# Optimization experiments

Measured on AMD Instinct MI355X. Metric: run time of the kernel, lower is better.

Reference implementation:

```python
import jax, jax.numpy as jnp
import numpy as np

NUM_HEADS = 16
EMBED_DIM = 1024
HEAD_DIM = EMBED_DIM // NUM_HEADS
DILATION = 4


def setup_inputs() -> dict:
    key = jax.random.key(0)
    ks = jax.random.split(key, 9)
    B, S, E = 2, 4096, EMBED_DIM
    scale = 1.0 / np.sqrt(E)
    inp = {
        "x": jax.random.normal(ks[0], (B, S, E), dtype=jnp.float32),
        "Wq": jax.random.normal(ks[1], (E, E), dtype=jnp.float32) * scale,
        "bq": jnp.zeros((E,), dtype=jnp.float32),
        "Wk": jax.random.normal(ks[2], (E, E), dtype=jnp.float32) * scale,
        "bk": jnp.zeros((E,), dtype=jnp.float32),
        "Wv": jax.random.normal(ks[3], (E, E), dtype=jnp.float32) * scale,
        "bv": jnp.zeros((E,), dtype=jnp.float32),
        "Wo": jax.random.normal(ks[4], (E, E), dtype=jnp.float32) * scale,
        "bo": jnp.zeros((E,), dtype=jnp.float32),
    }
    return inp


def reference(x, Wq, bq, Wk, bk, Wv, bv, Wo, bo):
    B, S, E = x.shape
    H, D = NUM_HEADS, HEAD_DIM

    def split_heads(t):  # [B,S,E] -> [B,H,S,D]
        return t.reshape(B, S, H, D).transpose(0, 2, 1, 3)

    q = split_heads(x @ Wq + bq)
    k = split_heads(x @ Wk + bk)[:, :, ::DILATION, :]   # dilated keys
    v = split_heads(x @ Wv + bv)[:, :, ::DILATION, :]   # dilated values

    scores = jnp.einsum('bhqd,bhkd->bhqk', q, k) / np.sqrt(D).astype(x.dtype)
    attn = jax.nn.softmax(scores, axis=-1)
    ctx = jnp.einsum('bhqk,bhkd->bhqd', attn, v)
    ctx = ctx.transpose(0, 2, 1, 3).reshape(B, S, E)
    return ctx @ Wo + bo
```

## Files before the change

kernel.cpp:

```cpp
#include <hip/hip_runtime.h>
#include <cstdint>
#include <cstddef>

typedef unsigned short u16;
typedef __attribute__((ext_vector_type(4))) float f32x4;
typedef __attribute__((ext_vector_type(8))) short short8;
typedef __attribute__((ext_vector_type(4))) unsigned short u16x4;

#define NH 16
#define ED 1024
#define HD 64
#define SEQ 4096
#define SKV 1024

__device__ __forceinline__ u16 f2bf(float f) {
  unsigned u = __builtin_bit_cast(unsigned, f);
  u += 0x7fffu + ((u >> 16) & 1u);
  return (u16)(u >> 16);
}

__device__ __forceinline__ void gload16(const void* g, void* l) {
  __builtin_amdgcn_global_load_lds((const __attribute__((address_space(1))) void*)g,
                                   (__attribute__((address_space(3))) void*)l, 16, 0, 0);
}

__device__ __forceinline__ f32x4 mfma16(short8 a, short8 b, f32x4 c) {
  return __builtin_amdgcn_mfma_f32_16x16x32_bf16(a, b, c, 0, 0, 0);
}

__global__ __launch_bounds__(256) void prep_kernel(
    const float* __restrict__ x, u16* __restrict__ x16,
    const float* __restrict__ Wq, const float* __restrict__ Wk,
    const float* __restrict__ Wv, const float* __restrict__ Wo,
    u16* __restrict__ Wqt, u16* __restrict__ Wkt,
    u16* __restrict__ Wvt, u16* __restrict__ Wot) {
  __shared__ float t[64][65];
  int bx = blockIdx.x;
  if (bx < 8192) {
    int i = bx * 256 + threadIdx.x;
    f32x4 v = ((const f32x4*)x)[i];
    u16x4 o;
#pragma unroll
    for (int j = 0; j < 4; ++j) o[j] = f2bf(v[j]);
    ((u16x4*)x16)[i] = o;
    return;
  }
  int tt = bx - 8192;
  int wi = tt >> 8;
  tt &= 255;
  const float* W = (wi == 0) ? Wq : (wi == 1) ? Wk : (wi == 2) ? Wv : Wo;
  u16* Wt = (wi == 0) ? Wqt : (wi == 1) ? Wkt : (wi == 2) ? Wvt : Wot;
  int kb = (tt >> 4) * 64, nb = (tt & 15) * 64;
  int tx = threadIdx.x & 15, ty = threadIdx.x >> 4;
#pragma unroll
  for (int j = 0; j < 4; ++j) {
    int row = ty + j * 16;
    f32x4 v = *(const f32x4*)&W[(size_t)(kb + row) * ED + nb + tx * 4];
#pragma unroll
    for (int i = 0; i < 4; ++i) t[row][tx * 4 + i] = v[i];
  }
  __syncthreads();
#pragma unroll
  for (int j = 0; j < 4; ++j) {
    int n = ty + j * 16;
    u16x4 o;
#pragma unroll
    for (int i = 0; i < 4; ++i) o[i] = f2bf(t[tx * 4 + i][n]);
    *(u16x4*)&Wt[(size_t)(nb + n) * ED + kb + tx * 4] = o;
  }
}

__global__ __launch_bounds__(256) void qkv_gemm(
    const u16* __restrict__ A,
    const u16* __restrict__ Wqt, const u16* __restrict__ Wkt, const u16* __restrict__ Wvt,
    const float* __restrict__ bq, const float* __restrict__ bk, const float* __restrict__ bv,
    u16* __restrict__ Q16, u16* __restrict__ K16, u16* __restrict__ VT16) {
  __shared__ u16 Al[128 * 32];
  __shared__ u16 Bl[128 * 32];
  const int tid = threadIdx.x;
  const int w = tid >> 6, lane = tid & 63;
  const int by = blockIdx.y;
  int which, mblk;
  if (by < 64) { which = 0; mblk = by; }
  else if (by < 80) { which = 1; mblk = by - 64; }
  else { which = 2; mblk = by - 80; }
  const int rowmult = (which == 0) ? 1 : 4;
  const u16* Bt = (which == 0) ? Wqt : (which == 1) ? Wkt : Wvt;
  const float* bias = (which == 0) ? bq : (which == 1) ? bk : bv;
  const int m0 = mblk * 128, n0 = blockIdx.x * 128;
  const int wr = w >> 1, wc = w & 1;
  f32x4 acc[4][4];
#pragma unroll
  for (int i = 0; i < 4; ++i)
#pragma unroll
    for (int j = 0; j < 4; ++j) acc[i][j] = (f32x4){0.f, 0.f, 0.f, 0.f};

  const int srow = w * 16 + (lane >> 2);
  const int scol = (lane & 3) * 8;
  const u16* Ag0 = A + (size_t)(m0 + srow) * rowmult * ED + scol;
  const u16* Ag1 = A + (size_t)(m0 + srow + 64) * rowmult * ED + scol;
  const u16* Bg0 = Bt + (size_t)(n0 + srow) * ED + scol;
  const u16* Bg1 = Bt + (size_t)(n0 + srow + 64) * ED + scol;
  u16* Al0 = &Al[(w * 16) * 32];
  u16* Al1 = &Al[(64 + w * 16) * 32];
  u16* Bl0 = &Bl[(w * 16) * 32];
  u16* Bl1 = &Bl[(64 + w * 16) * 32];

  for (int k0 = 0; k0 < ED; k0 += 32) {
    gload16(Ag0 + k0, Al0);
    gload16(Ag1 + k0, Al1);
    gload16(Bg0 + k0, Bl0);
    gload16(Bg1 + k0, Bl1);
    __syncthreads();
    short8 af[4], bfr[4];
#pragma unroll
    for (int i = 0; i < 4; ++i)
      af[i] = *(const short8*)&Al[(wr * 64 + i * 16 + (lane & 15)) * 32 + (lane >> 4) * 8];
#pragma unroll
    for (int i = 0; i < 4; ++i)
      bfr[i] = *(const short8*)&Bl[(wc * 64 + i * 16 + (lane & 15)) * 32 + (lane >> 4) * 8];
#pragma unroll
    for (int i = 0; i < 4; ++i)
#pragma unroll
      for (int j = 0; j < 4; ++j)
        acc[i][j] = mfma16(af[i], bfr[j], acc[i][j]);
    __syncthreads();
  }

  const int r0 = m0 + wr * 64, c0g = n0 + wc * 64;
  if (which == 0 || which == 1) {
    u16* o = (which == 0) ? Q16 : K16;
    const int sxlog2 = (which == 0) ? 12 : 10;
    const int Sx = 1 << sxlog2;
#pragma unroll
    for (int i = 0; i < 4; ++i) {
#pragma unroll
      for (int j = 0; j < 4; ++j) {
        int Cc = c0g + j * 16 + (lane & 15);
        int h = Cc >> 6, d = Cc & 63;
        float bv2 = bias[Cc];
#pragma unroll
        for (int r = 0; r < 4; ++r) {
          int R = r0 + i * 16 + (lane >> 4) * 4 + r;
          int b = R >> sxlog2, s = R & (Sx - 1);
          o[(((size_t)b * NH + h) * Sx + s) * HD + d] = f2bf(acc[i][j][r] + bv2);
        }
      }
    }
  } else {
    u16* o = VT16;
#pragma unroll
    for (int i = 0; i < 4; ++i) {
#pragma unroll
      for (int j = 0; j < 4; ++j) {
        int Cc = c0g + j * 16 + (lane & 15);
        int h = Cc >> 6, d = Cc & 63;
        float bv2 = bias[Cc];
#pragma unroll
        for (int r = 0; r < 4; ++r) {
          int R = r0 + i * 16 + (lane >> 4) * 4 + r;
          int b = R >> 10, s = R & 1023;
          o[(((size_t)b * NH + h) * HD + d) * SKV + s] = f2bf(acc[i][j][r] + bv2);
        }
      }
    }
  }
}

__global__ __launch_bounds__(256) void out_gemm(const u16* __restrict__ A,
                                                const u16* __restrict__ Bt,
                                                const float* __restrict__ bias,
                                                float* __restrict__ o) {
  __shared__ u16 Al[128 * 32];
  __shared__ u16 Bl[128 * 32];
  const int tid = threadIdx.x;
  const int w = tid >> 6, lane = tid & 63;
  const int m0 = blockIdx.y * 128, n0 = blockIdx.x * 128;
  const int wr = w >> 1, wc = w & 1;
  f32x4 acc[4][4];
#pragma unroll
  for (int i = 0; i < 4; ++i)
#pragma unroll
    for (int j = 0; j < 4; ++j) acc[i][j] = (f32x4){0.f, 0.f, 0.f, 0.f};

  const int srow = w * 16 + (lane >> 2);
  const int scol = (lane & 3) * 8;
  const u16* Ag0 = A + (size_t)(m0 + srow) * ED + scol;
  const u16* Ag1 = A + (size_t)(m0 + srow + 64) * ED + scol;
  const u16* Bg0 = Bt + (size_t)(n0 + srow) * ED + scol;
  const u16* Bg1 = Bt + (size_t)(n0 + srow + 64) * ED + scol;
  u16* Al0 = &Al[(w * 16) * 32];
  u16* Al1 = &Al[(64 + w * 16) * 32];
  u16* Bl0 = &Bl[(w * 16) * 32];
  u16* Bl1 = &Bl[(64 + w * 16) * 32];

  for (int k0 = 0; k0 < ED; k0 += 32) {
    gload16(Ag0 + k0, Al0);
    gload16(Ag1 + k0, Al1);
    gload16(Bg0 + k0, Bl0);
    gload16(Bg1 + k0, Bl1);
    __syncthreads();
    short8 af[4], bfr[4];
#pragma unroll
    for (int i = 0; i < 4; ++i)
      af[i] = *(const short8*)&Al[(wr * 64 + i * 16 + (lane & 15)) * 32 + (lane >> 4) * 8];
#pragma unroll
    for (int i = 0; i < 4; ++i)
      bfr[i] = *(const short8*)&Bl[(wc * 64 + i * 16 + (lane & 15)) * 32 + (lane >> 4) * 8];
#pragma unroll
    for (int i = 0; i < 4; ++i)
#pragma unroll
      for (int j = 0; j < 4; ++j)
        acc[i][j] = mfma16(af[i], bfr[j], acc[i][j]);
    __syncthreads();
  }

  const int r0 = m0 + wr * 64, c0g = n0 + wc * 64;
#pragma unroll
  for (int i = 0; i < 4; ++i) {
#pragma unroll
    for (int j = 0; j < 4; ++j) {
      int Cc = c0g + j * 16 + (lane & 15);
      float bv2 = bias[Cc];
#pragma unroll
      for (int r = 0; r < 4; ++r) {
        int R = r0 + i * 16 + (lane >> 4) * 4 + r;
        o[(size_t)R * ED + Cc] = acc[i][j][r] + bv2;
      }
    }
  }
}

__global__ __launch_bounds__(256) void attn_kernel(const u16* __restrict__ Q,
                                                   const u16* __restrict__ K,
                                                   const u16* __restrict__ VT,
                                                   u16* __restrict__ ctx) {
  __shared__ u16 Kl[2][64 * 64];
  __shared__ u16 Vl[2][64 * 64];
  __shared__ u16 Pl[4 * 16 * 64];
  const int tid = threadIdx.x, w = tid >> 6, lane = tid & 63;
  const int qt = blockIdx.x, bh = blockIdx.y, b = bh >> 4, h = bh & 15;

  const u16* Qp = Q + ((size_t)bh * SEQ + qt * 64 + w * 16) * HD;
  short8 qf0 = *(const short8*)&Qp[(lane & 15) * HD + (lane >> 4) * 8];
  short8 qf1 = *(const short8*)&Qp[(lane & 15) * HD + (lane >> 4) * 8 + 32];
  const u16* Kb = K + (size_t)bh * SKV * HD;
  const u16* VTb = VT + (size_t)bh * HD * SKV;

  float lp[4];
  f32x4 cacc[4];
#pragma unroll
  for (int r = 0; r < 4; ++r) lp[r] = 0.f;
#pragma unroll
  for (int i = 0; i < 4; ++i) cacc[i] = (f32x4){0.f, 0.f, 0.f, 0.f};

  const int srow = lane >> 3;
  const int scolswz = ((lane & 7) ^ (lane >> 3)) * 8;
  const int g4 = lane >> 4;
  const int sw7 = lane & 7;

  auto stage = [&](int buf, int kt) {
    gload16(Kb + ((size_t)kt * 64 + w * 8 + srow) * HD + scolswz, &Kl[buf][(w * 8) * 64]);
    gload16(Kb + ((size_t)kt * 64 + 32 + w * 8 + srow) * HD + scolswz, &Kl[buf][(32 + w * 8) * 64]);
    gload16(VTb + (size_t)(w * 8 + srow) * SKV + kt * 64 + scolswz, &Vl[buf][(w * 8) * 64]);
    gload16(VTb + (size_t)(32 + w * 8 + srow) * SKV + kt * 64 + scolswz, &Vl[buf][(32 + w * 8) * 64]);
  };

  stage(0, 0);
  const float SCL = 0.125f * 1.44269504f;
  u16* Pw = &Pl[w * 1024];

  for (int kt = 0; kt < 16; ++kt) {
    const int cur = kt & 1;
    __syncthreads();
    if (kt < 15) stage(cur ^ 1, kt + 1);
    const u16* Kc = Kl[cur];
    const u16* Vc = Vl[cur];

    f32x4 sv[4];
#pragma unroll
    for (int fk = 0; fk < 4; ++fk) {
      const int kr = fk * 16 + (lane & 15);
      short8 b0 = *(const short8*)&Kc[kr * 64 + ((g4 ^ sw7) * 8)];
      short8 b1 = *(const short8*)&Kc[kr * 64 + (((g4 + 4) ^ sw7) * 8)];
      f32x4 z = (f32x4){0.f, 0.f, 0.f, 0.f};
      z = mfma16(qf0, b0, z);
      z = mfma16(qf1, b1, z);
      sv[fk] = z;
    }

#pragma unroll
    for (int fk = 0; fk < 4; ++fk) {
#pragma unroll
      for (int r = 0; r < 4; ++r) {
        float p = exp2f(sv[fk][r] * SCL);
        lp[r] += p;
        int q = (lane >> 4) * 4 + r;
        int c = (lane & 15) + 16 * fk;
        Pw[q * 64 + (c ^ ((q & 7) * 8))] = f2bf(p);
      }
    }

    short8 pa0 = *(const short8*)&Pw[(lane & 15) * 64 + ((g4 ^ sw7) * 8)];
    short8 pa1 = *(const short8*)&Pw[(lane & 15) * 64 + (((g4 + 4) ^ sw7) * 8)];
#pragma unroll
    for (int fd = 0; fd < 4; ++fd) {
      const int vrow = fd * 16 + (lane & 15);
      short8 vb0 = *(const short8*)&Vc[vrow * 64 + ((g4 ^ sw7) * 8)];
      short8 vb1 = *(const short8*)&Vc[vrow * 64 + (((g4 + 4) ^ sw7) * 8)];
      cacc[fd] = mfma16(pa0, vb0, cacc[fd]);
      cacc[fd] = mfma16(pa1, vb1, cacc[fd]);
    }
  }

#pragma unroll
  for (int r = 0; r < 4; ++r) {
#pragma unroll
    for (int msk = 1; msk < 16; msk <<= 1) lp[r] += __shfl_xor(lp[r], msk);
  }

  const int q0 = qt * 64 + w * 16 + (lane >> 4) * 4;
#pragma unroll
  for (int r = 0; r < 4; ++r) {
    float inv = 1.f / lp[r];
#pragma unroll
    for (int fd = 0; fd < 4; ++fd) {
      int d = fd * 16 + (lane & 15);
      ctx[((size_t)b * SEQ + q0 + r) * ED + h * HD + d] = f2bf(cacc[fd][r] * inv);
    }
  }
}

extern "C" void kernel_launch(void* const* d_in, const int* in_sizes, int n_in,
                              void* d_out, int out_size, void* d_ws, size_t ws_size,
                              hipStream_t stream) {
  (void)in_sizes; (void)n_in; (void)out_size; (void)ws_size;
  const float* x  = (const float*)d_in[0];
  const float* Wq = (const float*)d_in[1];
  const float* bq = (const float*)d_in[2];
  const float* Wk = (const float*)d_in[3];
  const float* bk = (const float*)d_in[4];
  const float* Wv = (const float*)d_in[5];
  const float* bv = (const float*)d_in[6];
  const float* Wo = (const float*)d_in[7];
  const float* bo = (const float*)d_in[8];

  char* ws = (char*)d_ws;
  u16* x16 = (u16*)(ws);
  u16* Wqt = (u16*)(ws + (16ull << 20));
  u16* Wkt = (u16*)(ws + (18ull << 20));
  u16* Wvt = (u16*)(ws + (20ull << 20));
  u16* Wot = (u16*)(ws + (22ull << 20));
  u16* Q16 = (u16*)(ws + (24ull << 20));
  u16* K16 = (u16*)(ws + (40ull << 20));
  u16* VT16 = (u16*)(ws + (44ull << 20));
  u16* ctx16 = x16;

  prep_kernel<<<9216, 256, 0, stream>>>(x, x16, Wq, Wk, Wv, Wo, Wqt, Wkt, Wvt, Wot);

  qkv_gemm<<<dim3(8, 96), 256, 0, stream>>>(x16, Wqt, Wkt, Wvt, bq, bk, bv,
                                            Q16, K16, VT16);

  attn_kernel<<<dim3(64, 32), 256, 0, stream>>>(Q16, K16, VT16, ctx16);

  out_gemm<<<dim3(8, 64), 256, 0, stream>>>(ctx16, Wot, bo, (float*)d_out);
}
```

Baseline: 253.3 us.

## Fold softmax scale into Q, transpose score MFMA, pack P writes

The Q projection epilogue now premultiplies Q by the softmax scale times log2(e), so the attention loop can call a raw v_exp_f32 without a multiply. The score MFMA swaps operands so each lane holds four keys for one query. This lets the probabilities be packed into bf16 pairs with v_cvt_pk_bf16_f32 and written to LDS as 8-byte stores, and lets the row-sum reduce with two shuffles instead of per-row 16-lane reductions. s_setprio hints are added around the MFMA sections. The changes cut VALU and LDS-store work in the softmax, at the cost of slightly different rounding from scaling Q before the bf16 conversion.

Result: faster. 237.2 us (-6.3%).

```diff
diff --git a/kernel.cpp b/kernel.cpp
--- a/kernel.cpp
+++ b/kernel.cpp
@@ -6,6 +6,8 @@
 typedef __attribute__((ext_vector_type(4))) float f32x4;
 typedef __attribute__((ext_vector_type(8))) short short8;
 typedef __attribute__((ext_vector_type(4))) unsigned short u16x4;
+typedef short8 __attribute__((may_alias)) short8_a;
+typedef uint2 __attribute__((may_alias)) uint2_a;
 
 #define NH 16
 #define ED 1024
@@ -13,10 +15,24 @@
 #define SEQ 4096
 #define SKV 1024
 
+#define QSCALE 0.1803368801111204f
+
 __device__ __forceinline__ u16 f2bf(float f) {
   unsigned u = __builtin_bit_cast(unsigned, f);
   u += 0x7fffu + ((u >> 16) & 1u);
   return (u16)(u >> 16);
+}
+
+__device__ __forceinline__ float fexp2(float x) {
+  float r;
+  asm("v_exp_f32 %0, %1" : "=v"(r) : "v"(x));
+  return r;
+}
+
+__device__ __forceinline__ unsigned cvtpk(float lo, float hi) {
+  unsigned r;
+  asm("v_cvt_pk_bf16_f32 %0, %1, %2" : "=v"(r) : "v"(lo), "v"(hi));
+  return r;
 }
 
 __device__ __forceinline__ void gload16(const void* g, void* l) {
@@ -132,6 +148,7 @@
     u16* o = (which == 0) ? Q16 : K16;
     const int sxlog2 = (which == 0) ? 12 : 10;
     const int Sx = 1 << sxlog2;
+    const float scl = (which == 0) ? QSCALE : 1.0f;
 #pragma unroll
     for (int i = 0; i < 4; ++i) {
 #pragma unroll
@@ -143,7 +160,7 @@
         for (int r = 0; r < 4; ++r) {
           int R = r0 + i * 16 + (lane >> 4) * 4 + r;
           int b = R >> sxlog2, s = R & (Sx - 1);
-          o[(((size_t)b * NH + h) * Sx + s) * HD + d] = f2bf(acc[i][j][r] + bv2);
+          o[(((size_t)b * NH + h) * Sx + s) * HD + d] = f2bf((acc[i][j][r] + bv2) * scl);
         }
       }
     }
@@ -242,15 +259,13 @@
   const int qt = blockIdx.x, bh = blockIdx.y, b = bh >> 4, h = bh & 15;
 
   const u16* Qp = Q + ((size_t)bh * SEQ + qt * 64 + w * 16) * HD;
-  short8 qf0 = *(const short8*)&Qp[(lane & 15) * HD + (lane >> 4) * 8];
-  short8 qf1 = *(const short8*)&Qp[(lane & 15) * HD + (lane >> 4) * 8 + 32];
+  short8 qf0 = *(const short8_a*)&Qp[(lane & 15) * HD + (lane >> 4) * 8];
+  short8 qf1 = *(const short8_a*)&Qp[(lane & 15) * HD + (lane >> 4) * 8 + 32];
   const u16* Kb = K + (size_t)bh * SKV * HD;
   const u16* VTb = VT + (size_t)bh * HD * SKV;
 
-  float lp[4];
+  float lp = 0.f;
   f32x4 cacc[4];
-#pragma unroll
-  for (int r = 0; r < 4; ++r) lp[r] = 0.f;
 #pragma unroll
   for (int i = 0; i < 4; ++i) cacc[i] = (f32x4){0.f, 0.f, 0.f, 0.f};
 
@@ -258,6 +273,14 @@
   const int scolswz = ((lane & 7) ^ (lane >> 3)) * 8;
   const int g4 = lane >> 4;
   const int sw7 = lane & 7;
+  const int q = lane & 15;
+
+  int poff[4];
+#pragma unroll
+  for (int fk = 0; fk < 4; ++fk) {
+    int gr = 2 * fk + (g4 >> 1);
+    poff[fk] = q * 64 + ((gr ^ sw7) * 8) + 4 * (g4 & 1);
+  }
 
   auto stage = [&](int buf, int kt) {
     gload16(Kb + ((size_t)kt * 64 + w * 8 + srow) * HD + scolswz, &Kl[buf][(w * 8) * 64]);
@@ -267,7 +290,6 @@
   };
 
   stage(0, 0);
-  const float SCL = 0.125f * 1.44269504f;
   u16* Pw = &Pl[w * 1024];
 
   for (int kt = 0; kt < 16; ++kt) {
@@ -278,51 +300,53 @@
     const u16* Vc = Vl[cur];
 
     f32x4 sv[4];
+    __builtin_amdgcn_s_setprio(1);
 #pragma unroll
     for (int fk = 0; fk < 4; ++fk) {
       const int kr = fk * 16 + (lane & 15);
-      short8 b0 = *(const short8*)&Kc[kr * 64 + ((g4 ^ sw7) * 8)];
-      short8 b1 = *(const short8*)&Kc[kr * 64 + (((g4 + 4) ^ sw7) * 8)];
+      short8 a0 = *(const short8_a*)&Kc[kr * 64 + ((g4 ^ sw7) * 8)];
+      short8 a1 = *(const short8_a*)&Kc[kr * 64 + (((g4 + 4) ^ sw7) * 8)];
       f32x4 z = (f32x4){0.f, 0.f, 0.f, 0.f};
-      z = mfma16(qf0, b0, z);
-      z = mfma16(qf1, b1, z);
+      z = mfma16(a0, qf0, z);
+      z = mfma16(a1, qf1, z);
       sv[fk] = z;
     }
+    __builtin_amdgcn_s_setprio(0);
 
 #pragma unroll
     for (int fk = 0; fk < 4; ++fk) {
-#pragma unroll
-      for (int r = 0; r < 4; ++r) {
-        float p = exp2f(sv[fk][r] * SCL);
-        lp[r] += p;
-        int q = (lane >> 4) * 4 + r;
-        int c = (lane & 15) + 16 * fk;
-        Pw[q * 64 + (c ^ ((q & 7) * 8))] = f2bf(p);
-      }
-    }
-
-    short8 pa0 = *(const short8*)&Pw[(lane & 15) * 64 + ((g4 ^ sw7) * 8)];
-    short8 pa1 = *(const short8*)&Pw[(lane & 15) * 64 + (((g4 + 4) ^ sw7) * 8)];
+      float p0 = fexp2(sv[fk][0]);
+      float p1 = fexp2(sv[fk][1]);
+      float p2 = fexp2(sv[fk][2]);
+      float p3 = fexp2(sv[fk][3]);
+      lp += (p0 + p1) + (p2 + p3);
+      uint2 pk;
+      pk.x = cvtpk(p0, p1);
+      pk.y = cvtpk(p2, p3);
+      *(uint2_a*)&Pw[poff[fk]] = pk;
+    }
+
+    short8 pa0 = *(const short8_a*)&Pw[(lane & 15) * 64 + ((g4 ^ sw7) * 8)];
+    short8 pa1 = *(const short8_a*)&Pw[(lane & 15) * 64 + (((g4 + 4) ^ sw7) * 8)];
+    __builtin_amdgcn_s_setprio(1);
 #pragma unroll
     for (int fd = 0; fd < 4; ++fd) {
       const int vrow = fd * 16 + (lane & 15);
-      short8 vb0 = *(const short8*)&Vc[vrow * 64 + ((g4 ^ sw7) * 8)];
-      short8 vb1 = *(const short8*)&Vc[vrow * 64 + (((g4 + 4) ^ sw7) * 8)];
+      short8 vb0 = *(const short8_a*)&Vc[vrow * 64 + ((g4 ^ sw7) * 8)];
+      short8 vb1 = *(const short8_a*)&Vc[vrow * 64 + (((g4 + 4) ^ sw7) * 8)];
       cacc[fd] = mfma16(pa0, vb0, cacc[fd]);
       cacc[fd] = mfma16(pa1, vb1, cacc[fd]);
     }
-  }
-
+    __builtin_amdgcn_s_setprio(0);
+  }
+
+  lp += __shfl_xor(lp, 16);
+  lp += __shfl_xor(lp, 32);
+
+  const int q0 = qt * 64 + w * 16 + (lane >> 4) * 4;
 #pragma unroll
   for (int r = 0; r < 4; ++r) {
-#pragma unroll
-    for (int msk = 1; msk < 16; msk <<= 1) lp[r] += __shfl_xor(lp[r], msk);
-  }
-
-  const int q0 = qt * 64 + w * 16 + (lane >> 4) * 4;
-#pragma unroll
-  for (int r = 0; r < 4; ++r) {
-    float inv = 1.f / lp[r];
+    float inv = 1.f / __shfl(lp, (lane >> 4) * 4 + r);
 #pragma unroll
     for (int fd = 0; fd < 4; ++fd) {
       int d = fd * 16 + (lane & 15);
```
